# Performance work log

Hardware: AMD Instinct MI355X
Metric: run time of the kernel (lower is better)

Reference implementation:

```python
import jax, jax.numpy as jnp
import numpy as np

B, NQ, NK, DQ, DK, DV, H = 8, 256, 512, 256, 256, 256, 64
NEG = -1e6


def setup_inputs() -> dict:
    key = jax.random.key(0)
    k1, k2, k3, k4, k5, k6, k7 = jax.random.split(key, 7)
    return {
        "queries": jax.random.normal(k1, (B, NQ, DQ), dtype=jnp.float32),
        "keys": jax.random.normal(k2, (B, NK, DK), dtype=jnp.float32),
        "values": jax.random.normal(k3, (B, NK, DV), dtype=jnp.float32),
        "valid_lens": jax.random.randint(k4, (B,), 1, NK + 1),
        "Wq": jax.random.normal(k5, (DQ, H), dtype=jnp.float32) / np.sqrt(DQ),
        "Wk": jax.random.normal(k6, (DK, H), dtype=jnp.float32) / np.sqrt(DK),
        "wv": jax.random.normal(k7, (H,), dtype=jnp.float32) / np.sqrt(H),
    }


def reference(queries, keys, values, valid_lens, Wq, Wk, wv):
    # project: [B,NQ,H], [B,NK,H]
    q = jnp.einsum("bqd,dh->bqh", queries, Wq)
    k = jnp.einsum("bkd,dh->bkh", keys, Wk)
    # additive features: [B,NQ,NK,H] -> tanh -> reduce with w_v -> scores [B,NQ,NK]
    features = jnp.tanh(q[:, :, None, :] + k[:, None, :, :])
    scores = jnp.einsum("bqkh,h->bqk", features, wv)
    # masked softmax over key axis (per-batch valid_lens)
    mask = jnp.arange(NK)[None, None, :] < valid_lens[:, None, None]
    scores = jnp.where(mask, scores, NEG)
    attn = jax.nn.softmax(scores, axis=-1)
    # dropout p=0 (eval) -> identity; weighted sum of values [B,NQ,DV]
    return jnp.einsum("bqk,bkv->bqv", attn, values)
```

## Files before the change

### kernel.cpp

```cpp
#include <hip/hip_runtime.h>
#include <hip/hip_bf16.h>

constexpr int B  = 8;
constexpr int NQ = 256;
constexpr int NK = 512;
constexpr int D  = 256;
constexpr int DV = 256;
constexpr int H  = 64;
constexpr float NEG = -1e6f;
constexpr float LOG2E = 1.4426950408889634f;

__global__ __launch_bounds__(256) void proj_kernel(
    const float* __restrict__ queries, const float* __restrict__ keys,
    const float* __restrict__ Wq, const float* __restrict__ Wk,
    float* __restrict__ qp, float* __restrict__ kp)
{
    const int r0 = blockIdx.x * 4;
    const bool isQ = (r0 < B * NQ);
    const float* src = isQ ? queries + (size_t)r0 * D
                           : keys + (size_t)(r0 - B * NQ) * D;
    const float* W   = isQ ? Wq : Wk;
    float* out       = isQ ? qp + (size_t)r0 * H
                           : kp + (size_t)(r0 - B * NQ) * H;

    __shared__ __align__(16) float rows[4][D];
    ((float4*)&rows[0][0])[threadIdx.x] = ((const float4*)src)[threadIdx.x];
    __syncthreads();

    const int r = threadIdx.x >> 6;
    const int h = threadIdx.x & 63;
    float s = 0.f;
#pragma unroll 4
    for (int d4 = 0; d4 < D / 4; ++d4) {
        float4 rv = *(const float4*)&rows[r][d4 * 4];
        s = fmaf(rv.x, W[(d4 * 4 + 0) * H + h], s);
        s = fmaf(rv.y, W[(d4 * 4 + 1) * H + h], s);
        s = fmaf(rv.z, W[(d4 * 4 + 2) * H + h], s);
        s = fmaf(rv.w, W[(d4 * 4 + 3) * H + h], s);
    }
    out[r * H + h] = s;
}

constexpr int KT   = 128;
constexpr int KPAD = 68;

__global__ __launch_bounds__(256) void attn_kernel(
    const float* __restrict__ qp, const float* __restrict__ kp,
    const float* __restrict__ values, const int* __restrict__ valid_lens,
    const float* __restrict__ wv, float* __restrict__ out)
{
    const int b  = blockIdx.x >> 6;
    const int q0 = (blockIdx.x & 63) * 4;
    const int t  = threadIdx.x;
    const int w  = t >> 6;
    const int l  = t & 63;

    __shared__ __align__(16) float kT[KT * KPAD];
    __shared__ __align__(16) float qv[4][H];
    __shared__ __align__(16) float w2[H];
    __shared__ __align__(16) float sc[4][NK];

    qv[w][l] = qp[((size_t)b * NQ + q0 + w) * H + l];

    const float wvl = wv[l];
    float swv = wvl;
#pragma unroll
    for (int off = 32; off > 0; off >>= 1) swv += __shfl_xor(swv, off);
    if (w == 0) w2[l] = -2.f * wvl;

    const int vlen = valid_lens[b];

    for (int kt = 0; kt < NK / KT; ++kt) {
        if (kt * KT < vlen) {
            __syncthreads();
            const float* src = kp + ((size_t)b * NK + kt * KT) * H;
#pragma unroll
            for (int j = 0; j < 8; ++j) {
                int idx4 = t + j * 256;
                int kk = idx4 >> 4;
                int hb = (idx4 & 15) * 4;
                float4 v = ((const float4*)src)[idx4];
                *(float4*)&kT[kk * KPAD + hb] = v;
            }
            __syncthreads();

            const float* qrow = &qv[w][0];
            const float* k0r = &kT[l * KPAD];
            const float* k1r = &kT[(l + 64) * KPAD];
            float s0 = 0.f, s1 = 0.f;
#pragma unroll
            for (int h4 = 0; h4 < H / 4; ++h4) {
                float4 qq = *(const float4*)&qrow[h4 * 4];
                float4 ww = *(const float4*)&w2[h4 * 4];
                float4 k0 = *(const float4*)&k0r[h4 * 4];
                float4 k1 = *(const float4*)&k1r[h4 * 4];
                const float C = 2.f * LOG2E;
                float r;
                r = __builtin_amdgcn_rcpf(__builtin_amdgcn_exp2f((qq.x + k0.x) * C) + 1.f);
                s0 = fmaf(ww.x, r, s0);
                r = __builtin_amdgcn_rcpf(__builtin_amdgcn_exp2f((qq.y + k0.y) * C) + 1.f);
                s0 = fmaf(ww.y, r, s0);
                r = __builtin_amdgcn_rcpf(__builtin_amdgcn_exp2f((qq.z + k0.z) * C) + 1.f);
                s0 = fmaf(ww.z, r, s0);
                r = __builtin_amdgcn_rcpf(__builtin_amdgcn_exp2f((qq.w + k0.w) * C) + 1.f);
                s0 = fmaf(ww.w, r, s0);
                r = __builtin_amdgcn_rcpf(__builtin_amdgcn_exp2f((qq.x + k1.x) * C) + 1.f);
                s1 = fmaf(ww.x, r, s1);
                r = __builtin_amdgcn_rcpf(__builtin_amdgcn_exp2f((qq.y + k1.y) * C) + 1.f);
                s1 = fmaf(ww.y, r, s1);
                r = __builtin_amdgcn_rcpf(__builtin_amdgcn_exp2f((qq.z + k1.z) * C) + 1.f);
                s1 = fmaf(ww.z, r, s1);
                r = __builtin_amdgcn_rcpf(__builtin_amdgcn_exp2f((qq.w + k1.w) * C) + 1.f);
                s1 = fmaf(ww.w, r, s1);
            }
            int kg0 = kt * KT + l;
            int kg1 = kt * KT + l + 64;
            sc[w][kg0] = (kg0 < vlen) ? (s0 + swv) : NEG;
            sc[w][kg1] = (kg1 < vlen) ? (s1 + swv) : NEG;
        } else {
            sc[w][kt * KT + l]      = NEG;
            sc[w][kt * KT + l + 64] = NEG;
        }
    }

    float vals[8];
    float m = -INFINITY;
#pragma unroll
    for (int j = 0; j < 8; ++j) {
        vals[j] = sc[w][l + j * 64];
        m = fmaxf(m, vals[j]);
    }
#pragma unroll
    for (int off = 32; off > 0; off >>= 1) m = fmaxf(m, __shfl_xor(m, off));
    float sum = 0.f;
#pragma unroll
    for (int j = 0; j < 8; ++j) {
        float p = __builtin_amdgcn_exp2f((vals[j] - m) * LOG2E);
        vals[j] = p;
        sum += p;
    }
#pragma unroll
    for (int off = 32; off > 0; off >>= 1) sum += __shfl_xor(sum, off);
    const float rinv = __builtin_amdgcn_rcpf(sum);
#pragma unroll
    for (int j = 0; j < 8; ++j) sc[w][l + j * 64] = vals[j] * rinv;

    float4 acc = {0.f, 0.f, 0.f, 0.f};
    const float* Vb = values + (size_t)b * NK * DV;
    for (int k = 0; k < vlen; ++k) {
        float a = sc[w][k];
        float4 vv = *(const float4*)&Vb[(size_t)k * DV + 4 * l];
        acc.x = fmaf(a, vv.x, acc.x);
        acc.y = fmaf(a, vv.y, acc.y);
        acc.z = fmaf(a, vv.z, acc.z);
        acc.w = fmaf(a, vv.w, acc.w);
    }
    *(float4*)&out[((size_t)b * NQ + q0 + w) * DV + 4 * l] = acc;
}

extern "C" void kernel_launch(void* const* d_in, const int* in_sizes, int n_in,
                              void* d_out, int out_size, void* d_ws, size_t ws_size,
                              hipStream_t stream) {
    const float* queries    = (const float*)d_in[0];
    const float* keys       = (const float*)d_in[1];
    const float* values     = (const float*)d_in[2];
    const int*   valid_lens = (const int*)d_in[3];
    const float* Wq         = (const float*)d_in[4];
    const float* Wk         = (const float*)d_in[5];
    const float* wv         = (const float*)d_in[6];
    float* out = (float*)d_out;

    float* qp = (float*)d_ws;
    float* kp = qp + (size_t)B * NQ * H;

    proj_kernel<<<(B * NQ + B * NK) / 4, 256, 0, stream>>>(
        queries, keys, Wq, Wk, qp, kp);

    attn_kernel<<<B * (NQ / 4), 256, 0, stream>>>(
        qp, kp, values, valid_lens, wv, out);
}
```

Before: 121.3 us.

## Split key ranges across eight waves and share value loads among four queries

The attention kernel moves to 512 threads. Each pair of waves computes the scores for one query, one half of the keys each. In the weighted sum, each wave takes a 64-key slice and accumulates all four queries at once, so each value row is loaded once per block rather than once per query. The eight per-wave partial outputs are reduced through shared memory, which reuses the key tile buffer. The projection kernel now handles 8 rows per block so each weight load feeds two rows. The cost is extra block-wide syncs, a shared-memory reduction step, and the softmax being computed redundantly by both waves of each query.

```diff
diff --git a/kernel.cpp b/kernel.cpp
--- a/kernel.cpp
+++ b/kernel.cpp
@@ -10,12 +10,14 @@
 constexpr float NEG = -1e6f;
 constexpr float LOG2E = 1.4426950408889634f;
 
+constexpr int RPB = 8;
+
 __global__ __launch_bounds__(256) void proj_kernel(
     const float* __restrict__ queries, const float* __restrict__ keys,
     const float* __restrict__ Wq, const float* __restrict__ Wk,
     float* __restrict__ qp, float* __restrict__ kp)
 {
-    const int r0 = blockIdx.x * 4;
+    const int r0 = blockIdx.x * RPB;
     const bool isQ = (r0 < B * NQ);
     const float* src = isQ ? queries + (size_t)r0 * D
                            : keys + (size_t)(r0 - B * NQ) * D;
@@ -23,44 +25,60 @@
     float* out       = isQ ? qp + (size_t)r0 * H
                            : kp + (size_t)(r0 - B * NQ) * H;
 
-    __shared__ __align__(16) float rows[4][D];
-    ((float4*)&rows[0][0])[threadIdx.x] = ((const float4*)src)[threadIdx.x];
-    __syncthreads();
-
-    const int r = threadIdx.x >> 6;
+    __shared__ __align__(16) float rows[RPB][D];
+#pragma unroll
+    for (int j = 0; j < 2; ++j)
+        ((float4*)&rows[0][0])[threadIdx.x + j * 256] =
+            ((const float4*)src)[threadIdx.x + j * 256];
+    __syncthreads();
+
     const int h = threadIdx.x & 63;
-    float s = 0.f;
-#pragma unroll 4
+    const int g = threadIdx.x >> 6;
+    float s0 = 0.f, s1 = 0.f;
+#pragma unroll 2
     for (int d4 = 0; d4 < D / 4; ++d4) {
-        float4 rv = *(const float4*)&rows[r][d4 * 4];
-        s = fmaf(rv.x, W[(d4 * 4 + 0) * H + h], s);
-        s = fmaf(rv.y, W[(d4 * 4 + 1) * H + h], s);
-        s = fmaf(rv.z, W[(d4 * 4 + 2) * H + h], s);
-        s = fmaf(rv.w, W[(d4 * 4 + 3) * H + h], s);
-    }
-    out[r * H + h] = s;
+        float w0 = W[(d4 * 4 + 0) * H + h];
+        float w1 = W[(d4 * 4 + 1) * H + h];
+        float w2 = W[(d4 * 4 + 2) * H + h];
+        float w3 = W[(d4 * 4 + 3) * H + h];
+        float4 ra = *(const float4*)&rows[g][d4 * 4];
+        float4 rb = *(const float4*)&rows[g + 4][d4 * 4];
+        s0 = fmaf(ra.x, w0, s0);  s1 = fmaf(rb.x, w0, s1);
+        s0 = fmaf(ra.y, w1, s0);  s1 = fmaf(rb.y, w1, s1);
+        s0 = fmaf(ra.z, w2, s0);  s1 = fmaf(rb.z, w2, s1);
+        s0 = fmaf(ra.w, w3, s0);  s1 = fmaf(rb.w, w3, s1);
+    }
+    out[g * H + h]       = s0;
+    out[(g + 4) * H + h] = s1;
 }
 
 constexpr int KT   = 128;
 constexpr int KPAD = 68;
 
-__global__ __launch_bounds__(256) void attn_kernel(
+#define FMA4(acc, a, v) \
+    acc.x = fmaf(a, v.x, acc.x); acc.y = fmaf(a, v.y, acc.y); \
+    acc.z = fmaf(a, v.z, acc.z); acc.w = fmaf(a, v.w, acc.w);
+
+__global__ __launch_bounds__(512, 4) void attn_kernel(
     const float* __restrict__ qp, const float* __restrict__ kp,
     const float* __restrict__ values, const int* __restrict__ valid_lens,
     const float* __restrict__ wv, float* __restrict__ out)
 {
-    const int b  = blockIdx.x >> 6;
-    const int q0 = (blockIdx.x & 63) * 4;
-    const int t  = threadIdx.x;
-    const int w  = t >> 6;
-    const int l  = t & 63;
+    const int b    = blockIdx.x >> 6;
+    const int q0   = (blockIdx.x & 63) * 4;
+    const int t    = threadIdx.x;
+    const int w    = t >> 6;
+    const int l    = t & 63;
+    const int qloc = w >> 1;
+    const int half = w & 1;
 
     __shared__ __align__(16) float kT[KT * KPAD];
     __shared__ __align__(16) float qv[4][H];
     __shared__ __align__(16) float w2[H];
     __shared__ __align__(16) float sc[4][NK];
 
-    qv[w][l] = qp[((size_t)b * NQ + q0 + w) * H + l];
+    if (half == 0)
+        qv[qloc][l] = qp[((size_t)b * NQ + q0 + qloc) * H + l];
 
     const float wvl = wv[l];
     float swv = wvl;
@@ -71,12 +89,13 @@
     const int vlen = valid_lens[b];
 
     for (int kt = 0; kt < NK / KT; ++kt) {
+        const int kg = kt * KT + half * 64 + l;
         if (kt * KT < vlen) {
             __syncthreads();
             const float* src = kp + ((size_t)b * NK + kt * KT) * H;
 #pragma unroll
-            for (int j = 0; j < 8; ++j) {
-                int idx4 = t + j * 256;
+            for (int j = 0; j < 4; ++j) {
+                int idx4 = t + j * 512;
                 int kk = idx4 >> 4;
                 int hb = (idx4 & 15) * 4;
                 float4 v = ((const float4*)src)[idx4];
@@ -84,50 +103,37 @@
             }
             __syncthreads();
 
-            const float* qrow = &qv[w][0];
-            const float* k0r = &kT[l * KPAD];
-            const float* k1r = &kT[(l + 64) * KPAD];
-            float s0 = 0.f, s1 = 0.f;
+            const float* qrow = &qv[qloc][0];
+            const float* krow = &kT[(half * 64 + l) * KPAD];
+            float s0 = 0.f;
 #pragma unroll
             for (int h4 = 0; h4 < H / 4; ++h4) {
                 float4 qq = *(const float4*)&qrow[h4 * 4];
                 float4 ww = *(const float4*)&w2[h4 * 4];
-                float4 k0 = *(const float4*)&k0r[h4 * 4];
-                float4 k1 = *(const float4*)&k1r[h4 * 4];
+                float4 kk = *(const float4*)&krow[h4 * 4];
                 const float C = 2.f * LOG2E;
                 float r;
-                r = __builtin_amdgcn_rcpf(__builtin_amdgcn_exp2f((qq.x + k0.x) * C) + 1.f);
+                r = __builtin_amdgcn_rcpf(__builtin_amdgcn_exp2f((qq.x + kk.x) * C) + 1.f);
                 s0 = fmaf(ww.x, r, s0);
-                r = __builtin_amdgcn_rcpf(__builtin_amdgcn_exp2f((qq.y + k0.y) * C) + 1.f);
+                r = __builtin_amdgcn_rcpf(__builtin_amdgcn_exp2f((qq.y + kk.y) * C) + 1.f);
                 s0 = fmaf(ww.y, r, s0);
-                r = __builtin_amdgcn_rcpf(__builtin_amdgcn_exp2f((qq.z + k0.z) * C) + 1.f);
+                r = __builtin_amdgcn_rcpf(__builtin_amdgcn_exp2f((qq.z + kk.z) * C) + 1.f);
                 s0 = fmaf(ww.z, r, s0);
-                r = __builtin_amdgcn_rcpf(__builtin_amdgcn_exp2f((qq.w + k0.w) * C) + 1.f);
+                r = __builtin_amdgcn_rcpf(__builtin_amdgcn_exp2f((qq.w + kk.w) * C) + 1.f);
                 s0 = fmaf(ww.w, r, s0);
-                r = __builtin_amdgcn_rcpf(__builtin_amdgcn_exp2f((qq.x + k1.x) * C) + 1.f);
-                s1 = fmaf(ww.x, r, s1);
-                r = __builtin_amdgcn_rcpf(__builtin_amdgcn_exp2f((qq.y + k1.y) * C) + 1.f);
-                s1 = fmaf(ww.y, r, s1);
-                r = __builtin_amdgcn_rcpf(__builtin_amdgcn_exp2f((qq.z + k1.z) * C) + 1.f);
-                s1 = fmaf(ww.z, r, s1);
-                r = __builtin_amdgcn_rcpf(__builtin_amdgcn_exp2f((qq.w + k1.w) * C) + 1.f);
-                s1 = fmaf(ww.w, r, s1);
             }
-            int kg0 = kt * KT + l;
-            int kg1 = kt * KT + l + 64;
-            sc[w][kg0] = (kg0 < vlen) ? (s0 + swv) : NEG;
-            sc[w][kg1] = (kg1 < vlen) ? (s1 + swv) : NEG;
+            sc[qloc][kg] = (kg < vlen) ? (s0 + swv) : NEG;
         } else {
-            sc[w][kt * KT + l]      = NEG;
-            sc[w][kt * KT + l + 64] = NEG;
+            sc[qloc][kg] = NEG;
         }
     }
+    __syncthreads();
 
     float vals[8];
     float m = -INFINITY;
 #pragma unroll
     for (int j = 0; j < 8; ++j) {
-        vals[j] = sc[w][l + j * 64];
+        vals[j] = sc[qloc][l + j * 64];
         m = fmaxf(m, vals[j]);
     }
 #pragma unroll
@@ -142,20 +148,57 @@
 #pragma unroll
     for (int off = 32; off > 0; off >>= 1) sum += __shfl_xor(sum, off);
     const float rinv = __builtin_amdgcn_rcpf(sum);
-#pragma unroll
-    for (int j = 0; j < 8; ++j) sc[w][l + j * 64] = vals[j] * rinv;
-
-    float4 acc = {0.f, 0.f, 0.f, 0.f};
+    if (half == 0) {
+        sc[qloc][l + 0 * 64] = vals[0] * rinv;
+        sc[qloc][l + 1 * 64] = vals[1] * rinv;
+        sc[qloc][l + 2 * 64] = vals[2] * rinv;
+        sc[qloc][l + 3 * 64] = vals[3] * rinv;
+    } else {
+        sc[qloc][l + 4 * 64] = vals[4] * rinv;
+        sc[qloc][l + 5 * 64] = vals[5] * rinv;
+        sc[qloc][l + 6 * 64] = vals[6] * rinv;
+        sc[qloc][l + 7 * 64] = vals[7] * rinv;
+    }
+    __syncthreads();
+
+    float4 acc0 = {0,0,0,0}, acc1 = {0,0,0,0}, acc2 = {0,0,0,0}, acc3 = {0,0,0,0};
     const float* Vb = values + (size_t)b * NK * DV;
-    for (int k = 0; k < vlen; ++k) {
-        float a = sc[w][k];
-        float4 vv = *(const float4*)&Vb[(size_t)k * DV + 4 * l];
-        acc.x = fmaf(a, vv.x, acc.x);
-        acc.y = fmaf(a, vv.y, acc.y);
-        acc.z = fmaf(a, vv.z, acc.z);
-        acc.w = fmaf(a, vv.w, acc.w);
-    }
-    *(float4*)&out[((size_t)b * NQ + q0 + w) * DV + 4 * l] = acc;
+    const int kbeg = w * 64;
+    const int kend = min(vlen - kbeg, 64);
+    const int kcnt = (kend > 0) ? ((kend + 3) >> 2) : 0;
+    for (int c = 0; c < kcnt; ++c) {
+        const int k = kbeg + 4 * c;
+        float4 a0 = *(const float4*)&sc[0][k];
+        float4 a1 = *(const float4*)&sc[1][k];
+        float4 a2 = *(const float4*)&sc[2][k];
+        float4 a3 = *(const float4*)&sc[3][k];
+        const float* vr = Vb + (size_t)k * DV + 4 * l;
+        float4 v0 = *(const float4*)(vr);
+        float4 v1 = *(const float4*)(vr + DV);
+        float4 v2 = *(const float4*)(vr + 2 * DV);
+        float4 v3 = *(const float4*)(vr + 3 * DV);
+        FMA4(acc0, a0.x, v0); FMA4(acc0, a0.y, v1); FMA4(acc0, a0.z, v2); FMA4(acc0, a0.w, v3);
+        FMA4(acc1, a1.x, v0); FMA4(acc1, a1.y, v1); FMA4(acc1, a1.z, v2); FMA4(acc1, a1.w, v3);
+        FMA4(acc2, a2.x, v0); FMA4(acc2, a2.y, v1); FMA4(acc2, a2.z, v2); FMA4(acc2, a2.w, v3);
+        FMA4(acc3, a3.x, v0); FMA4(acc3, a3.y, v1); FMA4(acc3, a3.z, v2); FMA4(acc3, a3.w, v3);
+    }
+
+    float* pt = kT;
+    *(float4*)&pt[(w * 4 + 0) * 256 + 4 * l] = acc0;
+    *(float4*)&pt[(w * 4 + 1) * 256 + 4 * l] = acc1;
+    *(float4*)&pt[(w * 4 + 2) * 256 + 4 * l] = acc2;
+    *(float4*)&pt[(w * 4 + 3) * 256 + 4 * l] = acc3;
+    __syncthreads();
+
+    if (w < 4) {
+        float4 r = {0,0,0,0};
+#pragma unroll
+        for (int s = 0; s < 8; ++s) {
+            float4 p = *(const float4*)&pt[(s * 4 + w) * 256 + 4 * l];
+            r.x += p.x; r.y += p.y; r.z += p.z; r.w += p.w;
+        }
+        *(float4*)&out[((size_t)b * NQ + q0 + w) * DV + 4 * l] = r;
+    }
 }
 
 extern "C" void kernel_launch(void* const* d_in, const int* in_sizes, int n_in,
@@ -173,9 +216,9 @@
     float* qp = (float*)d_ws;
     float* kp = qp + (size_t)B * NQ * H;
 
-    proj_kernel<<<(B * NQ + B * NK) / 4, 256, 0, stream>>>(
+    proj_kernel<<<(B * NQ + B * NK) / RPB, 256, 0, stream>>>(
         queries, keys, Wq, Wk, qp, kp);
 
-    attn_kernel<<<B * (NQ / 4), 256, 0, stream>>>(
+    attn_kernel<<<B * (NQ / 4), 512, 0, stream>>>(
         qp, kp, values, valid_lens, wv, out);
 }
```

Measured after the change: 105.5 us. -13.0%, faster.
